# Optimization experiments

Hardware: AMD Instinct MI355X
Metric: run time of the kernel (lower is better)

## Reference

```python
import jax, jax.numpy as jnp
import numpy as np
import math

N_HEAD = 16

def _c(a):
    # stack real/imag -> complex64
    return jax.lax.complex(a[..., 0], a[..., 1])

def _rope_phasor(T, D, dtype=jnp.float32):
    inv_freq = 1.0 / (10000.0 ** (jnp.arange(D, dtype=dtype) / D))
    t = jnp.arange(T, dtype=dtype)
    freqs = jnp.outer(t, inv_freq)  # [T, D]
    return jax.lax.complex(jnp.cos(freqs), jnp.sin(freqs))

def setup_inputs() -> dict:
    key = jax.random.key(0)
    ks = jax.random.split(key, 9)
    B, T, C = 2, 1024, 1024
    s = 0.02
    return {
        "x":  jax.random.normal(ks[0], (B, T, C, 2), jnp.float32),
        "wq": jax.random.normal(ks[1], (C, C, 2), jnp.float32) * s,
        "bq": jax.random.normal(ks[2], (C, 2), jnp.float32) * s,
        "wk": jax.random.normal(ks[3], (C, C, 2), jnp.float32) * s,
        "bk": jax.random.normal(ks[4], (C, 2), jnp.float32) * s,
        "wv": jax.random.normal(ks[5], (C, C, 2), jnp.float32) * s,
        "bv": jax.random.normal(ks[6], (C, 2), jnp.float32) * s,
        "wo": jax.random.normal(ks[7], (C, C, 2), jnp.float32) * s,
        "bo": jax.random.normal(ks[8], (C, 2), jnp.float32) * s,
    }

def reference(x, wq, bq, wk, bk, wv, bv, wo, bo):
    B, T, C, _ = x.shape
    H = N_HEAD
    D = C // H
    xc = _c(x)
    # complex linear projections: y = x @ W^T + b
    q = xc @ _c(wq).T + _c(bq)
    k = xc @ _c(wk).T + _c(bk)
    v = xc @ _c(wv).T + _c(bv)
    # [B, T, C] -> [B, H, T, D]
    q = q.reshape(B, T, H, D).transpose(0, 2, 1, 3)
    k = k.reshape(B, T, H, D).transpose(0, 2, 1, 3)
    v = v.reshape(B, T, H, D).transpose(0, 2, 1, 3)
    # complex RoPE phasor multiply
    ph = _rope_phasor(T, D)[None, None]  # [1,1,T,D]
    q = q * ph
    k = k * ph
    # complex QK^H, scaled
    score = jnp.einsum('bhtd,bhsd->bhts', q, jnp.conj(k)) / math.sqrt(D)
    # softmax over magnitude, then real-valued complex weights
    attn = jax.nn.softmax(jnp.abs(score), axis=-1)
    attn_c = jax.lax.complex(attn, jnp.zeros_like(attn))
    out = jnp.einsum('bhts,bhsd->bhtd', attn_c, v)
    out = out.transpose(0, 2, 1, 3).reshape(B, T, C)
    out = out @ _c(wo).T + _c(bo)
    # return real/imag stacked for a real-valued harness
    return jnp.stack([out.real, out.imag], axis=-1)
```

## Files before the change

kernel.cpp:

```cpp
#include <hip/hip_runtime.h>
#include <math.h>

#define T_SEQ  1024
#define C_DIM  1024
#define NH_    16
#define H_DIM  64
#define SCL    (0.125f * 1.4426950408889634f)

typedef __bf16 bf16;
typedef __bf16 bf16x4 __attribute__((ext_vector_type(4)));
typedef __bf16 bf16x8 __attribute__((ext_vector_type(8)));
typedef float  f32x4  __attribute__((ext_vector_type(4)));

#define MFMA16(a, b, c) __builtin_amdgcn_mfma_f32_16x16x32_bf16(a, b, c, 0, 0, 0)

#define GLOAD_LDS16(g, l) __builtin_amdgcn_global_load_lds( \
    (const __attribute__((address_space(1))) void*)(g),     \
    (__attribute__((address_space(3))) void*)(l), 16, 0, 0)

__device__ __forceinline__ bf16x8 neg8(bf16x8 x) {
    union { bf16x8 v; unsigned int u[4]; } t;
    t.v = x;
    t.u[0] ^= 0x80008000u; t.u[1] ^= 0x80008000u;
    t.u[2] ^= 0x80008000u; t.u[3] ^= 0x80008000u;
    return t.v;
}

__device__ __forceinline__ bf16x8 frag_sw(const bf16* plane, int row, int chunk) {
    int c = chunk ^ (row & 7);
    return *(const bf16x8*)&plane[row * 64 + c * 8];
}
__device__ __forceinline__ bf16x8 frag_sw4(const bf16* plane, int row, int chunk) {
    int c = chunk ^ (row & 3);
    return *(const bf16x8*)&plane[row * 32 + c * 8];
}

__global__ __launch_bounds__(256)
void split_all(const float* __restrict__ x,  const float* __restrict__ wq,
               const float* __restrict__ wk, const float* __restrict__ wv,
               const float* __restrict__ wo,
               bf16* Xr, bf16* Xi, bf16* Wqr, bf16* Wqi, bf16* Wkr, bf16* Wki,
               bf16* Wvr, bf16* Wvi, bf16* Wor, bf16* Woi,
               float* __restrict__ rope)
{
    int z = blockIdx.y;
    if (z == 5) {
        if (blockIdx.x >= 256) return;
        int idx = blockIdx.x * 256 + threadIdx.x;
        int tp = idx >> 6, d = idx & 63;
        float invf = exp2f((float)d * -0.2076205059304601f);
        float fr = (float)tp * invf;
        float sn, cs; sincosf(fr, &sn, &cs);
        *(float2*)&rope[(size_t)idx * 2] = make_float2(cs, sn);
        return;
    }
    if (z > 0 && blockIdx.x >= 512) return;
    const float* in; bf16 *pr, *pi;
    if      (z == 0) { in = x;  pr = Xr;  pi = Xi;  }
    else if (z == 1) { in = wq; pr = Wqr; pi = Wqi; }
    else if (z == 2) { in = wk; pr = Wkr; pi = Wki; }
    else if (z == 3) { in = wv; pr = Wvr; pi = Wvi; }
    else             { in = wo; pr = Wor; pi = Woi; }
    int idx = (blockIdx.x * 256 + threadIdx.x) * 8;
    bf16x8 r, im;
#pragma unroll
    for (int j = 0; j < 4; j++) {
        float4 v = *(const float4*)(in + (size_t)idx * 2 + j * 4);
        r[2*j]   = (bf16)v.x; im[2*j]   = (bf16)v.y;
        r[2*j+1] = (bf16)v.z; im[2*j+1] = (bf16)v.w;
    }
    *(bf16x8*)(pr + idx) = r;
    *(bf16x8*)(pi + idx) = im;
}

__device__ __forceinline__ void cgemm128(
    bf16* __restrict__ smem,
    const bf16* __restrict__ Ar, const bf16* __restrict__ Ai,
    const bf16* __restrict__ Br, const bf16* __restrict__ Bi,
    const float* __restrict__ bias, const float* __restrict__ rope,
    bf16* __restrict__ Yr, bf16* __restrict__ Yi, int m0, int n0, int mode)
{
    const int t = threadIdx.x, lane = t & 63, wave = t >> 6;
    const int wm = (wave >> 1) * 64, wn = (wave & 1) * 32;
    const int lm = lane & 15, quad = lane >> 4;
    const int s_lr = lane >> 3, s_c = (lane & 7) ^ s_lr;

    f32x4 accr[4][2], acci[4][2];
#pragma unroll
    for (int i = 0; i < 4; i++)
#pragma unroll
        for (int j = 0; j < 2; j++) { accr[i][j] = (f32x4)0.f; acci[i][j] = (f32x4)0.f; }

    for (int k0 = 0; k0 < C_DIM; k0 += 64) {
#pragma unroll
        for (int j = 0; j < 12; j++) {
            int c = wave + 4 * j;
            const bf16* src; bf16* dst;
            if (c < 16)      {             src = Ar + (size_t)(m0 + c * 8 + s_lr) * C_DIM + k0 + s_c * 8; dst = smem + c * 512; }
            else if (c < 32) { int u = c - 16; src = Ai + (size_t)(m0 + u * 8 + s_lr) * C_DIM + k0 + s_c * 8; dst = smem + 8192 + u * 512; }
            else if (c < 40) { int u = c - 32; src = Br + (size_t)(n0 + u * 8 + s_lr) * C_DIM + k0 + s_c * 8; dst = smem + 16384 + u * 512; }
            else             { int u = c - 40; src = Bi + (size_t)(n0 + u * 8 + s_lr) * C_DIM + k0 + s_c * 8; dst = smem + 20480 + u * 512; }
            GLOAD_LDS16(src, dst);
        }
        __syncthreads();

#pragma unroll
        for (int kh = 0; kh < 2; kh++) {
            bf16x8 ar[4], ai_[4], br_[2], bi_[2], bn_[2];
#pragma unroll
            for (int i = 0; i < 4; i++) {
                ar[i]  = frag_sw(smem,        wm + i * 16 + lm, kh * 4 + quad);
                ai_[i] = frag_sw(smem + 8192, wm + i * 16 + lm, kh * 4 + quad);
            }
#pragma unroll
            for (int j = 0; j < 2; j++) {
                br_[j] = frag_sw(smem + 16384, wn + j * 16 + lm, kh * 4 + quad);
                bi_[j] = frag_sw(smem + 20480, wn + j * 16 + lm, kh * 4 + quad);
                bn_[j] = neg8(bi_[j]);
            }
#pragma unroll
            for (int i = 0; i < 4; i++)
#pragma unroll
                for (int j = 0; j < 2; j++) {
                    accr[i][j] = MFMA16(ar[i],  br_[j], accr[i][j]);
                    accr[i][j] = MFMA16(ai_[i], bn_[j], accr[i][j]);
                    acci[i][j] = MFMA16(ar[i],  bi_[j], acci[i][j]);
                    acci[i][j] = MFMA16(ai_[i], br_[j], acci[i][j]);
                }
        }
        __syncthreads();
    }

    const int h = n0 >> 6, bb = m0 >> 10, tbase = m0 & (T_SEQ - 1);

    if (mode == 1) {
#pragma unroll
        for (int i = 0; i < 4; i++)
#pragma unroll
            for (int j = 0; j < 2; j++) {
                int d = wn + j * 16 + lm;
                float2 bv = *(const float2*)&bias[2 * (n0 + d)];
#pragma unroll
                for (int r = 0; r < 4; r++) {
                    int tpos = tbase + wm + i * 16 + quad * 4 + r;
                    float2 ph = *(const float2*)&rope[((size_t)tpos * H_DIM + d) * 2];
                    float yr = accr[i][j][r] + bv.x;
                    float yi = acci[i][j][r] + bv.y;
                    accr[i][j][r] = yr * ph.x - yi * ph.y;
                    acci[i][j][r] = yr * ph.y + yi * ph.x;
                }
            }
        bf16* dsts[2] = { Yr, Yi };
#pragma unroll
        for (int pass = 0; pass < 2; pass++) {
            __syncthreads();
#pragma unroll
            for (int i = 0; i < 4; i++)
#pragma unroll
                for (int j = 0; j < 2; j++)
#pragma unroll
                    for (int r = 0; r < 4; r++)
                        smem[(wm + i * 16 + quad * 4 + r) * 72 + wn + j * 16 + lm] =
                            (bf16)(pass ? acci[i][j][r] : accr[i][j][r]);
            __syncthreads();
            bf16* dst = dsts[pass] + ((size_t)(bb * NH_ + h) * T_SEQ + tbase) * H_DIM;
#pragma unroll
            for (int p = 0; p < 4; p++) {
                int ch = t + 256 * p;
                int row = ch >> 3, o = (ch & 7) * 8;
                *(bf16x8*)&dst[row * H_DIM + o] = *(const bf16x8*)&smem[row * 72 + o];
            }
        }
    } else {
        bf16* dsts[2] = { Yr, Yi };
#pragma unroll
        for (int pass = 0; pass < 2; pass++) {
            __syncthreads();
#pragma unroll
            for (int i = 0; i < 4; i++)
#pragma unroll
                for (int j = 0; j < 2; j++) {
                    int d = wn + j * 16 + lm;
                    float2 bv = *(const float2*)&bias[2 * (n0 + d)];
                    float bb2 = pass ? bv.y : bv.x;
                    bf16x4 pk;
#pragma unroll
                    for (int r = 0; r < 4; r++)
                        pk[r] = (bf16)((pass ? acci[i][j][r] : accr[i][j][r]) + bb2);
                    *(bf16x4*)&smem[d * 136 + wm + i * 16 + quad * 4] = pk;
                }
            __syncthreads();
            bf16* dst = dsts[pass] + ((size_t)(bb * NH_ + h) * H_DIM) * T_SEQ + tbase;
#pragma unroll
            for (int p = 0; p < 4; p++) {
                int ch = t + 256 * p;
                int row = ch >> 4, o = (ch & 15) * 8;
                *(bf16x8*)&dst[(size_t)row * T_SEQ + o] = *(const bf16x8*)&smem[row * 136 + o];
            }
        }
    }
}

__global__ __launch_bounds__(256, 3)
void qkv_gemm(const bf16* __restrict__ Xr, const bf16* __restrict__ Xi,
              const bf16* __restrict__ Wqr, const bf16* __restrict__ Wqi,
              const bf16* __restrict__ Wkr, const bf16* __restrict__ Wki,
              const bf16* __restrict__ Wvr, const bf16* __restrict__ Wvi,
              const float* __restrict__ bq, const float* __restrict__ bk,
              const float* __restrict__ bv, const float* __restrict__ rope,
              bf16* Qr, bf16* Qi, bf16* Kr, bf16* Ki, bf16* Vr, bf16* Vi)
{
    __shared__ __attribute__((aligned(16))) bf16 smem[24576];
    int m0 = blockIdx.y * 128, n0 = blockIdx.x * 64;
    const bf16 *Br, *Bi; const float* bias; bf16 *Yr, *Yi; int mode;
    if (blockIdx.z == 0)      { Br = Wqr; Bi = Wqi; bias = bq; Yr = Qr; Yi = Qi; mode = 1; }
    else if (blockIdx.z == 1) { Br = Wkr; Bi = Wki; bias = bk; Yr = Kr; Yi = Ki; mode = 1; }
    else                      { Br = Wvr; Bi = Wvi; bias = bv; Yr = Vr; Yi = Vi; mode = 2; }
    cgemm128(smem, Xr, Xi, Br, Bi, bias, rope, Yr, Yi, m0, n0, mode);
}

__global__ __launch_bounds__(256, 4)
void out_gemm(const bf16* __restrict__ Ar, const bf16* __restrict__ Ai,
              const bf16* __restrict__ Br, const bf16* __restrict__ Bi,
              const float* __restrict__ bias, float* __restrict__ Y)
{
    __shared__ __attribute__((aligned(16))) bf16 sm[16384];
    const int t = threadIdx.x, lane = t & 63, wave = t >> 6;
    const int lm = lane & 15, quad = lane >> 4;
    const int s_lr = lane >> 3, s_c = (lane & 7) ^ s_lr;
    const int wm = (wave >> 1) * 32, wn = (wave & 1) * 32;
    const int m0 = blockIdx.y * 64, n0 = blockIdx.x * 64;

    f32x4 accr[2][2], acci[2][2];
#pragma unroll
    for (int i = 0; i < 2; i++)
#pragma unroll
        for (int j = 0; j < 2; j++) { accr[i][j] = (f32x4)0.f; acci[i][j] = (f32x4)0.f; }

    for (int k0 = 0; k0 < C_DIM; k0 += 64) {
#pragma unroll
        for (int j = 0; j < 8; j++) {
            int c = wave + 4 * j;
            const bf16* src; bf16* dst;
            if (c < 8)       {             src = Ar + (size_t)(m0 + c * 8 + s_lr) * C_DIM + k0 + s_c * 8; dst = sm + c * 512; }
            else if (c < 16) { int u = c - 8;  src = Ai + (size_t)(m0 + u * 8 + s_lr) * C_DIM + k0 + s_c * 8; dst = sm + 4096 + u * 512; }
            else if (c < 24) { int u = c - 16; src = Br + (size_t)(n0 + u * 8 + s_lr) * C_DIM + k0 + s_c * 8; dst = sm + 8192 + u * 512; }
            else             { int u = c - 24; src = Bi + (size_t)(n0 + u * 8 + s_lr) * C_DIM + k0 + s_c * 8; dst = sm + 12288 + u * 512; }
            GLOAD_LDS16(src, dst);
        }
        __syncthreads();
#pragma unroll
        for (int kh = 0; kh < 2; kh++) {
            bf16x8 ar[2], ai_[2], br_[2], bi_[2], bn_[2];
#pragma unroll
            for (int i = 0; i < 2; i++) {
                ar[i]  = frag_sw(sm,        wm + i * 16 + lm, kh * 4 + quad);
                ai_[i] = frag_sw(sm + 4096, wm + i * 16 + lm, kh * 4 + quad);
            }
#pragma unroll
            for (int j = 0; j < 2; j++) {
                br_[j] = frag_sw(sm + 8192,  wn + j * 16 + lm, kh * 4 + quad);
                bi_[j] = frag_sw(sm + 12288, wn + j * 16 + lm, kh * 4 + quad);
                bn_[j] = neg8(bi_[j]);
            }
#pragma unroll
            for (int i = 0; i < 2; i++)
#pragma unroll
                for (int j = 0; j < 2; j++) {
                    accr[i][j] = MFMA16(ar[i],  br_[j], accr[i][j]);
                    accr[i][j] = MFMA16(ai_[i], bn_[j], accr[i][j]);
                    acci[i][j] = MFMA16(ar[i],  bi_[j], acci[i][j]);
                    acci[i][j] = MFMA16(ai_[i], br_[j], acci[i][j]);
                }
        }
        __syncthreads();
    }
#pragma unroll
    for (int i = 0; i < 2; i++)
#pragma unroll
        for (int j = 0; j < 2; j++) {
            int n = n0 + wn + j * 16 + lm;
            float2 bv = *(const float2*)&bias[2 * n];
#pragma unroll
            for (int r = 0; r < 4; r++) {
                int m = m0 + wm + i * 16 + quad * 4 + r;
                *(float2*)&Y[((size_t)m * C_DIM + n) * 2] =
                    make_float2(accr[i][j][r] + bv.x, acci[i][j][r] + bv.y);
            }
        }
}

__global__ __launch_bounds__(512, 4)
void attn_mfma(const bf16* __restrict__ Qpr, const bf16* __restrict__ Qpi,
               const bf16* __restrict__ Kpr, const bf16* __restrict__ Kpi,
               const bf16* __restrict__ Vtr, const bf16* __restrict__ Vti,
               bf16* __restrict__ ABr, bf16* __restrict__ ABi)
{
    __shared__ __attribute__((aligned(16))) bf16 smem[32768];
    const int t = threadIdx.x, lane = t & 63, w = t >> 6;
    const int qg = w & 3, sh = w >> 2;
    const int lm = lane & 15, quad = lane >> 4;
    const int q0 = blockIdx.x * 64;
    const int h = blockIdx.y, b = blockIdx.z;
    const size_t hb = (size_t)(b * NH_ + h) * T_SEQ * H_DIM;
    const int s_lr = lane >> 3, s_c = (lane & 7) ^ s_lr;
    const int lr4 = lane >> 2, sc4 = ((lane & 3) ^ (lr4 & 3)) * 8;

    {
        const bf16* gq = (sh ? Qpi : Qpr) + hb + (size_t)q0 * H_DIM;
        bf16* lq = smem + 16384 + sh * 4096;
#pragma unroll
        for (int j = 0; j < 2; j++) {
            int cc = qg * 2 + j;
            GLOAD_LDS16(gq + (cc * 8 + s_lr) * H_DIM + s_c * 8, lq + cc * 512);
        }
    }
    __syncthreads();

    bf16x8 qfr[2], qfi[2], nqfr[2];
#pragma unroll
    for (int kh = 0; kh < 2; kh++) {
        qfr[kh]  = frag_sw(smem + 16384, qg * 16 + lm, kh * 4 + quad);
        qfi[kh]  = frag_sw(smem + 20480, qg * 16 + lm, kh * 4 + quad);
        nqfr[kh] = neg8(qfr[kh]);
    }

#pragma unroll
    for (int pre = 0; pre < 1; pre++) {
        const int S = sh * 512;
        bf16* bd = smem + sh * 8192;
        if (qg < 2) {
            const bf16* g = (qg ? Kpi : Kpr) + hb + (size_t)S * H_DIM;
            bf16* d = bd + (qg ? 2048 : 0);
#pragma unroll
            for (int cc = 0; cc < 4; cc++)
                GLOAD_LDS16(g + (cc * 8 + s_lr) * H_DIM + s_c * 8, d + cc * 512);
        } else {
            const bf16* g = (qg == 2 ? Vtr : Vti) + hb + S;
            bf16* d = bd + (qg == 2 ? 4096 : 6144);
#pragma unroll
            for (int cc = 0; cc < 4; cc++)
                GLOAD_LDS16(g + (size_t)(cc * 16 + lr4) * T_SEQ + sc4, d + cc * 512);
        }
    }

    f32x4 Or[4], Oi[4];
#pragma unroll
    for (int nt = 0; nt < 4; nt++) { Or[nt] = (f32x4)0.f; Oi[nt] = (f32x4)0.f; }
    float lsum = 0.f;
    const int idxA = (((2 * quad) & 3) * 16 + lm) * 4;
    const int idxB = idxA + 64;
    const bool hisel = quad >= 2;

    for (int it = 0; it < 16; it++) {
        __syncthreads();
        if (it < 15) {
            const int S = (it + 1) * 32 + sh * 512;
            bf16* bd = smem + ((it + 1) & 1) * 16384 + sh * 8192;
            if (qg < 2) {
                const bf16* g = (qg ? Kpi : Kpr) + hb + (size_t)S * H_DIM;
                bf16* d = bd + (qg ? 2048 : 0);
#pragma unroll
                for (int cc = 0; cc < 4; cc++)
                    GLOAD_LDS16(g + (cc * 8 + s_lr) * H_DIM + s_c * 8, d + cc * 512);
            } else {
                const bf16* g = (qg == 2 ? Vtr : Vti) + hb + S;
                bf16* d = bd + (qg == 2 ? 4096 : 6144);
#pragma unroll
                for (int cc = 0; cc < 4; cc++)
                    GLOAD_LDS16(g + (size_t)(cc * 16 + lr4) * T_SEQ + sc4, d + cc * 512);
            }
        }
        const bf16* buf = smem + (it & 1) * 16384 + sh * 8192;

        union { unsigned int u[2]; bf16 b[4]; } pk[2];
#pragma unroll
        for (int ct = 0; ct < 2; ct++) {
            f32x4 sre = (f32x4)0.f, sim = (f32x4)0.f;
#pragma unroll
            for (int kh = 0; kh < 2; kh++) {
                bf16x8 kr = frag_sw(buf,        ct * 16 + lm, kh * 4 + quad);
                bf16x8 ki = frag_sw(buf + 2048, ct * 16 + lm, kh * 4 + quad);
                sre = MFMA16(kr, qfr[kh],  sre);
                sre = MFMA16(ki, qfi[kh],  sre);
                sim = MFMA16(kr, qfi[kh],  sim);
                sim = MFMA16(ki, nqfr[kh], sim);
            }
#pragma unroll
            for (int r = 0; r < 4; r++) {
                float p = exp2f(sqrtf(sre[r] * sre[r] + sim[r] * sim[r]) * SCL);
                lsum += p;
                pk[ct].b[r] = (bf16)p;
            }
        }

        union { unsigned int u[4]; bf16x8 v; } pf;
        {
            int a0 = __builtin_amdgcn_ds_bpermute(idxA, (int)pk[0].u[0]);
            int a1 = __builtin_amdgcn_ds_bpermute(idxA, (int)pk[1].u[0]);
            int b0 = __builtin_amdgcn_ds_bpermute(idxA, (int)pk[0].u[1]);
            int b1 = __builtin_amdgcn_ds_bpermute(idxA, (int)pk[1].u[1]);
            int c0 = __builtin_amdgcn_ds_bpermute(idxB, (int)pk[0].u[0]);
            int c1 = __builtin_amdgcn_ds_bpermute(idxB, (int)pk[1].u[0]);
            int d0 = __builtin_amdgcn_ds_bpermute(idxB, (int)pk[0].u[1]);
            int d1 = __builtin_amdgcn_ds_bpermute(idxB, (int)pk[1].u[1]);
            pf.u[0] = (unsigned int)(hisel ? a1 : a0);
            pf.u[1] = (unsigned int)(hisel ? b1 : b0);
            pf.u[2] = (unsigned int)(hisel ? c1 : c0);
            pf.u[3] = (unsigned int)(hisel ? d1 : d0);
        }

#pragma unroll
        for (int nt = 0; nt < 4; nt++) {
            Or[nt] = MFMA16(pf.v, frag_sw4(buf + 4096, nt * 16 + lm, quad), Or[nt]);
            Oi[nt] = MFMA16(pf.v, frag_sw4(buf + 6144, nt * 16 + lm, quad), Oi[nt]);
        }
    }

    lsum += __shfl_xor(lsum, 16);
    lsum += __shfl_xor(lsum, 32);

    __syncthreads();
    float* Of  = (float*)smem;
    float* lsc = Of + 128 * 66;
    if (sh == 1) {
#pragma unroll
        for (int nt = 0; nt < 4; nt++)
#pragma unroll
            for (int r = 0; r < 4; r++) {
                Of[((qg * 2 + 0) * 16 + quad * 4 + r) * 66 + nt * 16 + lm] = Or[nt][r];
                Of[((qg * 2 + 1) * 16 + quad * 4 + r) * 66 + nt * 16 + lm] = Oi[nt][r];
            }
        if (quad == 0) lsc[qg * 16 + lm] = lsum;
    }
    __syncthreads();
    if (sh == 0) {
        float ltot = lsum + lsc[qg * 16 + lm];
        float lv = 1.f / ltot;
        float linv[4];
#pragma unroll
        for (int r = 0; r < 4; r++)
            linv[r] = __shfl(lv, (quad << 4) + quad * 4 + r, 64);
        size_t mbase = (size_t)(b * T_SEQ + q0 + qg * 16 + quad * 4) * C_DIM;
        int colb = h * H_DIM + lm;
#pragma unroll
        for (int nt = 0; nt < 4; nt++)
#pragma unroll
            for (int r = 0; r < 4; r++) {
                float orv = Or[nt][r] + Of[((qg * 2 + 0) * 16 + quad * 4 + r) * 66 + nt * 16 + lm];
                float oiv = Oi[nt][r] + Of[((qg * 2 + 1) * 16 + quad * 4 + r) * 66 + nt * 16 + lm];
                size_t o = mbase + (size_t)r * C_DIM + colb + nt * 16;
                ABr[o] = (bf16)(orv * linv[r]);
                ABi[o] = (bf16)(oiv * linv[r]);
            }
    }
}

extern "C" void kernel_launch(void* const* d_in, const int* in_sizes, int n_in,
                              void* d_out, int out_size, void* d_ws, size_t ws_size,
                              hipStream_t stream) {
    const float* x  = (const float*)d_in[0];
    const float* wq = (const float*)d_in[1];
    const float* bq = (const float*)d_in[2];
    const float* wk = (const float*)d_in[3];
    const float* bk = (const float*)d_in[4];
    const float* wv = (const float*)d_in[5];
    const float* bv = (const float*)d_in[6];
    const float* wo = (const float*)d_in[7];
    const float* bo = (const float*)d_in[8];

    float* rope = (float*)d_ws;
    bf16* w = (bf16*)(rope + 131072);
    const size_t MSZ = (size_t)2048 * 1024;
    const size_t WSZ = (size_t)1024 * 1024;
    const size_t PSZ = (size_t)2 * NH_ * T_SEQ * H_DIM;

    bf16 *Xr = w, *Xi = Xr + MSZ;
    bf16 *Wqr = Xi + MSZ,  *Wqi = Wqr + WSZ;
    bf16 *Wkr = Wqi + WSZ, *Wki = Wkr + WSZ;
    bf16 *Wvr = Wki + WSZ, *Wvi = Wvr + WSZ;
    bf16 *Wor = Wvi + WSZ, *Woi = Wor + WSZ;
    bf16 *Qr = Woi + WSZ, *Qi = Qr + PSZ;
    bf16 *Kr = Qi + PSZ,  *Ki = Kr + PSZ;
    bf16 *Vr = Ki + PSZ,  *Vi = Vr + PSZ;
    bf16 *ABr = Vi + PSZ, *ABi = ABr + MSZ;

    split_all<<<dim3(1024, 6), 256, 0, stream>>>(x, wq, wk, wv, wo,
        Xr, Xi, Wqr, Wqi, Wkr, Wki, Wvr, Wvi, Wor, Woi, rope);

    qkv_gemm<<<dim3(16, 16, 3), 256, 0, stream>>>(
        Xr, Xi, Wqr, Wqi, Wkr, Wki, Wvr, Wvi, bq, bk, bv, rope,
        Qr, Qi, Kr, Ki, Vr, Vi);

    attn_mfma<<<dim3(16, 16, 2), 512, 0, stream>>>(
        Qr, Qi, Kr, Ki, Vr, Vi, ABr, ABi);

    out_gemm<<<dim3(16, 32), 256, 0, stream>>>(ABr, ABi, Wor, Woi, bo, (float*)d_out);
}
```

Baseline: 217.0 us.

## Restructure attention into smaller blocks with 16-key tiles and K16 MFMA for PV

The attention kernel goes from 512-thread blocks over 64 queries to 256-thread blocks over 32 queries, doubling the grid, and now streams 16-key tiles over 32 iterations instead of 32-key tiles. The P·V product uses the 16x16x16 bf16 MFMA, so the probability fragment from the score MFMA feeds it directly and the ds_bpermute shuffle goes away. The softmax scale is folded into the Q RoPE phasor in the QKV GEMM epilogue, removing a multiply per score. The trade-off is more barriers and loop iterations per block and half as much K/V reuse per load.

After: 234.7 us. 8.1% more time.

```diff
diff --git a/kernel.cpp b/kernel.cpp
--- a/kernel.cpp
+++ b/kernel.cpp
@@ -10,9 +10,11 @@
 typedef __bf16 bf16;
 typedef __bf16 bf16x4 __attribute__((ext_vector_type(4)));
 typedef __bf16 bf16x8 __attribute__((ext_vector_type(8)));
+typedef short  s16x4  __attribute__((ext_vector_type(4)));
 typedef float  f32x4  __attribute__((ext_vector_type(4)));
 
-#define MFMA16(a, b, c) __builtin_amdgcn_mfma_f32_16x16x32_bf16(a, b, c, 0, 0, 0)
+#define MFMA16(a, b, c)  __builtin_amdgcn_mfma_f32_16x16x32_bf16(a, b, c, 0, 0, 0)
+#define MFMAK16(a, b, c) __builtin_amdgcn_mfma_f32_16x16x16bf16_1k(a, b, c, 0, 0, 0)
 
 #define GLOAD_LDS16(g, l) __builtin_amdgcn_global_load_lds( \
     (const __attribute__((address_space(1))) void*)(g),     \
@@ -29,10 +31,6 @@
 __device__ __forceinline__ bf16x8 frag_sw(const bf16* plane, int row, int chunk) {
     int c = chunk ^ (row & 7);
     return *(const bf16x8*)&plane[row * 64 + c * 8];
-}
-__device__ __forceinline__ bf16x8 frag_sw4(const bf16* plane, int row, int chunk) {
-    int c = chunk ^ (row & 3);
-    return *(const bf16x8*)&plane[row * 32 + c * 8];
 }
 
 __global__ __launch_bounds__(256)
@@ -78,7 +76,8 @@
     const bf16* __restrict__ Ar, const bf16* __restrict__ Ai,
     const bf16* __restrict__ Br, const bf16* __restrict__ Bi,
     const float* __restrict__ bias, const float* __restrict__ rope,
-    bf16* __restrict__ Yr, bf16* __restrict__ Yi, int m0, int n0, int mode)
+    bf16* __restrict__ Yr, bf16* __restrict__ Yi, int m0, int n0, int mode,
+    float qscale)
 {
     const int t = threadIdx.x, lane = t & 63, wave = t >> 6;
     const int wm = (wave >> 1) * 64, wn = (wave & 1) * 32;
@@ -144,10 +143,11 @@
                 for (int r = 0; r < 4; r++) {
                     int tpos = tbase + wm + i * 16 + quad * 4 + r;
                     float2 ph = *(const float2*)&rope[((size_t)tpos * H_DIM + d) * 2];
+                    float px = ph.x * qscale, py = ph.y * qscale;
                     float yr = accr[i][j][r] + bv.x;
                     float yi = acci[i][j][r] + bv.y;
-                    accr[i][j][r] = yr * ph.x - yi * ph.y;
-                    acci[i][j][r] = yr * ph.y + yi * ph.x;
+                    accr[i][j][r] = yr * px - yi * py;
+                    acci[i][j][r] = yr * py + yi * px;
                 }
             }
         bf16* dsts[2] = { Yr, Yi };
@@ -212,11 +212,11 @@
 {
     __shared__ __attribute__((aligned(16))) bf16 smem[24576];
     int m0 = blockIdx.y * 128, n0 = blockIdx.x * 64;
-    const bf16 *Br, *Bi; const float* bias; bf16 *Yr, *Yi; int mode;
-    if (blockIdx.z == 0)      { Br = Wqr; Bi = Wqi; bias = bq; Yr = Qr; Yi = Qi; mode = 1; }
-    else if (blockIdx.z == 1) { Br = Wkr; Bi = Wki; bias = bk; Yr = Kr; Yi = Ki; mode = 1; }
-    else                      { Br = Wvr; Bi = Wvi; bias = bv; Yr = Vr; Yi = Vi; mode = 2; }
-    cgemm128(smem, Xr, Xi, Br, Bi, bias, rope, Yr, Yi, m0, n0, mode);
+    const bf16 *Br, *Bi; const float* bias; bf16 *Yr, *Yi; int mode; float qs;
+    if (blockIdx.z == 0)      { Br = Wqr; Bi = Wqi; bias = bq; Yr = Qr; Yi = Qi; mode = 1; qs = SCL;  }
+    else if (blockIdx.z == 1) { Br = Wkr; Bi = Wki; bias = bk; Yr = Kr; Yi = Ki; mode = 1; qs = 1.0f; }
+    else                      { Br = Wvr; Bi = Wvi; bias = bv; Yr = Vr; Yi = Vi; mode = 2; qs = 1.0f; }
+    cgemm128(smem, Xr, Xi, Br, Bi, bias, rope, Yr, Yi, m0, n0, mode, qs);
 }
 
 __global__ __launch_bounds__(256, 4)
@@ -290,153 +290,122 @@
         }
 }
 
-__global__ __launch_bounds__(512, 4)
+__global__ __launch_bounds__(256, 5)
 void attn_mfma(const bf16* __restrict__ Qpr, const bf16* __restrict__ Qpi,
                const bf16* __restrict__ Kpr, const bf16* __restrict__ Kpi,
                const bf16* __restrict__ Vtr, const bf16* __restrict__ Vti,
                bf16* __restrict__ ABr, bf16* __restrict__ ABi)
 {
-    __shared__ __attribute__((aligned(16))) bf16 smem[32768];
-    const int t = threadIdx.x, lane = t & 63, w = t >> 6;
-    const int qg = w & 3, sh = w >> 2;
+    __shared__ __attribute__((aligned(16))) bf16 smem[16384];
+    const int t = threadIdx.x, lane = t & 63, wv = t >> 6;
+    const int qg = wv & 1, sh = wv >> 1;
     const int lm = lane & 15, quad = lane >> 4;
-    const int q0 = blockIdx.x * 64;
+    const int q0 = blockIdx.x * 32;
     const int h = blockIdx.y, b = blockIdx.z;
     const size_t hb = (size_t)(b * NH_ + h) * T_SEQ * H_DIM;
     const int s_lr = lane >> 3, s_c = (lane & 7) ^ s_lr;
-    const int lr4 = lane >> 2, sc4 = ((lane & 3) ^ (lr4 & 3)) * 8;
-
-    {
-        const bf16* gq = (sh ? Qpi : Qpr) + hb + (size_t)q0 * H_DIM;
-        bf16* lq = smem + 16384 + sh * 4096;
-#pragma unroll
-        for (int j = 0; j < 2; j++) {
-            int cc = qg * 2 + j;
-            GLOAD_LDS16(gq + (cc * 8 + s_lr) * H_DIM + s_c * 8, lq + cc * 512);
-        }
+
+#pragma unroll
+    for (int j = 0; j < 2; j++) {
+        int u = wv * 2 + j;
+        const bf16* gq = ((u >> 2) ? Qpi : Qpr) + hb + (size_t)q0 * H_DIM;
+        GLOAD_LDS16(gq + ((u & 3) * 8 + s_lr) * H_DIM + s_c * 8,
+                    smem + 8192 + (u >> 2) * 2048 + (u & 3) * 512);
     }
     __syncthreads();
-
     bf16x8 qfr[2], qfi[2], nqfr[2];
 #pragma unroll
     for (int kh = 0; kh < 2; kh++) {
-        qfr[kh]  = frag_sw(smem + 16384, qg * 16 + lm, kh * 4 + quad);
-        qfi[kh]  = frag_sw(smem + 20480, qg * 16 + lm, kh * 4 + quad);
+        qfr[kh]  = frag_sw(smem + 8192,  qg * 16 + lm, kh * 4 + quad);
+        qfi[kh]  = frag_sw(smem + 10240, qg * 16 + lm, kh * 4 + quad);
         nqfr[kh] = neg8(qfr[kh]);
     }
 
-#pragma unroll
-    for (int pre = 0; pre < 1; pre++) {
-        const int S = sh * 512;
-        bf16* bd = smem + sh * 8192;
-        if (qg < 2) {
-            const bf16* g = (qg ? Kpi : Kpr) + hb + (size_t)S * H_DIM;
-            bf16* d = bd + (qg ? 2048 : 0);
-#pragma unroll
-            for (int cc = 0; cc < 4; cc++)
-                GLOAD_LDS16(g + (cc * 8 + s_lr) * H_DIM + s_c * 8, d + cc * 512);
-        } else {
-            const bf16* g = (qg == 2 ? Vtr : Vti) + hb + S;
-            bf16* d = bd + (qg == 2 ? 4096 : 6144);
-#pragma unroll
-            for (int cc = 0; cc < 4; cc++)
-                GLOAD_LDS16(g + (size_t)(cc * 16 + lr4) * T_SEQ + sc4, d + cc * 512);
-        }
+    const bf16 *g0, *g1; size_t cstride; int gstep, dof0, dof1;
+    if (qg == 0) {
+        size_t off = hb + (size_t)(sh * 512) * H_DIM + (size_t)s_lr * H_DIM + s_c * 8;
+        g0 = Kpr + off; g1 = Kpi + off;
+        cstride = (size_t)8 * H_DIM; gstep = 16 * H_DIM;
+        dof0 = sh * 4096; dof1 = sh * 4096 + 1024;
+    } else {
+        size_t off = hb + (size_t)(sh * 512) + (size_t)(lane >> 1) * T_SEQ + (lane & 1) * 8;
+        g0 = Vtr + off; g1 = Vti + off;
+        cstride = (size_t)32 * T_SEQ; gstep = 16;
+        dof0 = sh * 4096 + 2048; dof1 = sh * 4096 + 3072;
+    }
+#pragma unroll
+    for (int cc = 0; cc < 2; cc++) {
+        GLOAD_LDS16(g0 + cc * cstride, smem + dof0 + cc * 512);
+        GLOAD_LDS16(g1 + cc * cstride, smem + dof1 + cc * 512);
     }
 
     f32x4 Or[4], Oi[4];
 #pragma unroll
     for (int nt = 0; nt < 4; nt++) { Or[nt] = (f32x4)0.f; Oi[nt] = (f32x4)0.f; }
     float lsum = 0.f;
-    const int idxA = (((2 * quad) & 3) * 16 + lm) * 4;
-    const int idxB = idxA + 64;
-    const bool hisel = quad >= 2;
-
-    for (int it = 0; it < 16; it++) {
+
+    for (int it = 0; it < 32; it++) {
         __syncthreads();
-        if (it < 15) {
-            const int S = (it + 1) * 32 + sh * 512;
-            bf16* bd = smem + ((it + 1) & 1) * 16384 + sh * 8192;
-            if (qg < 2) {
-                const bf16* g = (qg ? Kpi : Kpr) + hb + (size_t)S * H_DIM;
-                bf16* d = bd + (qg ? 2048 : 0);
-#pragma unroll
-                for (int cc = 0; cc < 4; cc++)
-                    GLOAD_LDS16(g + (cc * 8 + s_lr) * H_DIM + s_c * 8, d + cc * 512);
-            } else {
-                const bf16* g = (qg == 2 ? Vtr : Vti) + hb + S;
-                bf16* d = bd + (qg == 2 ? 4096 : 6144);
-#pragma unroll
-                for (int cc = 0; cc < 4; cc++)
-                    GLOAD_LDS16(g + (size_t)(cc * 16 + lr4) * T_SEQ + sc4, d + cc * 512);
-            }
-        }
-        const bf16* buf = smem + (it & 1) * 16384 + sh * 8192;
-
-        union { unsigned int u[2]; bf16 b[4]; } pk[2];
-#pragma unroll
-        for (int ct = 0; ct < 2; ct++) {
-            f32x4 sre = (f32x4)0.f, sim = (f32x4)0.f;
-#pragma unroll
-            for (int kh = 0; kh < 2; kh++) {
-                bf16x8 kr = frag_sw(buf,        ct * 16 + lm, kh * 4 + quad);
-                bf16x8 ki = frag_sw(buf + 2048, ct * 16 + lm, kh * 4 + quad);
-                sre = MFMA16(kr, qfr[kh],  sre);
-                sre = MFMA16(ki, qfi[kh],  sre);
-                sim = MFMA16(kr, qfi[kh],  sim);
-                sim = MFMA16(ki, nqfr[kh], sim);
-            }
-#pragma unroll
-            for (int r = 0; r < 4; r++) {
-                float p = exp2f(sqrtf(sre[r] * sre[r] + sim[r] * sim[r]) * SCL);
-                lsum += p;
-                pk[ct].b[r] = (bf16)p;
-            }
-        }
-
-        union { unsigned int u[4]; bf16x8 v; } pf;
-        {
-            int a0 = __builtin_amdgcn_ds_bpermute(idxA, (int)pk[0].u[0]);
-            int a1 = __builtin_amdgcn_ds_bpermute(idxA, (int)pk[1].u[0]);
-            int b0 = __builtin_amdgcn_ds_bpermute(idxA, (int)pk[0].u[1]);
-            int b1 = __builtin_amdgcn_ds_bpermute(idxA, (int)pk[1].u[1]);
-            int c0 = __builtin_amdgcn_ds_bpermute(idxB, (int)pk[0].u[0]);
-            int c1 = __builtin_amdgcn_ds_bpermute(idxB, (int)pk[1].u[0]);
-            int d0 = __builtin_amdgcn_ds_bpermute(idxB, (int)pk[0].u[1]);
-            int d1 = __builtin_amdgcn_ds_bpermute(idxB, (int)pk[1].u[1]);
-            pf.u[0] = (unsigned int)(hisel ? a1 : a0);
-            pf.u[1] = (unsigned int)(hisel ? b1 : b0);
-            pf.u[2] = (unsigned int)(hisel ? c1 : c0);
-            pf.u[3] = (unsigned int)(hisel ? d1 : d0);
-        }
-
+        if (it < 31) {
+            const bf16* s0 = g0 + (size_t)(it + 1) * gstep;
+            const bf16* s1 = g1 + (size_t)(it + 1) * gstep;
+            bf16* d = smem + ((it + 1) & 1) * 8192;
+#pragma unroll
+            for (int cc = 0; cc < 2; cc++) {
+                GLOAD_LDS16(s0 + cc * cstride, d + dof0 + cc * 512);
+                GLOAD_LDS16(s1 + cc * cstride, d + dof1 + cc * 512);
+            }
+        }
+        const bf16* buf = smem + (it & 1) * 8192 + sh * 4096;
+
+        f32x4 sre = (f32x4)0.f, sim = (f32x4)0.f;
+#pragma unroll
+        for (int kh = 0; kh < 2; kh++) {
+            bf16x8 kr = frag_sw(buf,        lm, kh * 4 + quad);
+            bf16x8 ki = frag_sw(buf + 1024, lm, kh * 4 + quad);
+            sre = MFMA16(kr, qfr[kh],  sre);
+            sre = MFMA16(ki, qfi[kh],  sre);
+            sim = MFMA16(kr, qfi[kh],  sim);
+            sim = MFMA16(ki, nqfr[kh], sim);
+        }
+        union { s16x4 s; bf16x4 b; } pf;
+#pragma unroll
+        for (int r = 0; r < 4; r++) {
+            float p = exp2f(sqrtf(sre[r] * sre[r] + sim[r] * sim[r]));
+            lsum += p;
+            pf.b[r] = (bf16)p;
+        }
+
+        const bf16* vr = buf + 2048;
+        const bf16* vi = buf + 3072;
 #pragma unroll
         for (int nt = 0; nt < 4; nt++) {
-            Or[nt] = MFMA16(pf.v, frag_sw4(buf + 4096, nt * 16 + lm, quad), Or[nt]);
-            Oi[nt] = MFMA16(pf.v, frag_sw4(buf + 6144, nt * 16 + lm, quad), Oi[nt]);
+            s16x4 vfr = *(const s16x4*)&vr[(nt * 16 + lm) * 16 + quad * 4];
+            s16x4 vfi = *(const s16x4*)&vi[(nt * 16 + lm) * 16 + quad * 4];
+            Or[nt] = MFMAK16(pf.s, vfr, Or[nt]);
+            Oi[nt] = MFMAK16(pf.s, vfi, Oi[nt]);
         }
     }
 
     lsum += __shfl_xor(lsum, 16);
     lsum += __shfl_xor(lsum, 32);
 
+    float* Of = (float*)smem;
+    float* fm = Of + 4096;
     __syncthreads();
-    float* Of  = (float*)smem;
-    float* lsc = Of + 128 * 66;
     if (sh == 1) {
 #pragma unroll
         for (int nt = 0; nt < 4; nt++)
 #pragma unroll
             for (int r = 0; r < 4; r++) {
-                Of[((qg * 2 + 0) * 16 + quad * 4 + r) * 66 + nt * 16 + lm] = Or[nt][r];
-                Of[((qg * 2 + 1) * 16 + quad * 4 + r) * 66 + nt * 16 + lm] = Oi[nt][r];
-            }
-        if (quad == 0) lsc[qg * 16 + lm] = lsum;
+                Of[(qg * 16 + quad * 4 + r) * 64 + nt * 16 + lm]        = Or[nt][r];
+                Of[(32 + qg * 16 + quad * 4 + r) * 64 + nt * 16 + lm]   = Oi[nt][r];
+            }
+        if (quad == 0) fm[qg * 16 + lm] = lsum;
     }
     __syncthreads();
     if (sh == 0) {
-        float ltot = lsum + lsc[qg * 16 + lm];
-        float lv = 1.f / ltot;
+        float lv = 1.f / (lsum + fm[qg * 16 + lm]);
         float linv[4];
 #pragma unroll
         for (int r = 0; r < 4; r++)
@@ -447,8 +416,8 @@
         for (int nt = 0; nt < 4; nt++)
 #pragma unroll
             for (int r = 0; r < 4; r++) {
-                float orv = Or[nt][r] + Of[((qg * 2 + 0) * 16 + quad * 4 + r) * 66 + nt * 16 + lm];
-                float oiv = Oi[nt][r] + Of[((qg * 2 + 1) * 16 + quad * 4 + r) * 66 + nt * 16 + lm];
+                float orv = Or[nt][r] + Of[(qg * 16 + quad * 4 + r) * 64 + nt * 16 + lm];
+                float oiv = Oi[nt][r] + Of[(32 + qg * 16 + quad * 4 + r) * 64 + nt * 16 + lm];
                 size_t o = mbase + (size_t)r * C_DIM + colb + nt * 16;
                 ABr[o] = (bf16)(orv * linv[r]);
                 ABi[o] = (bf16)(oiv * linv[r]);
@@ -492,7 +461,7 @@
         Xr, Xi, Wqr, Wqi, Wkr, Wki, Wvr, Wvi, bq, bk, bv, rope,
         Qr, Qi, Kr, Ki, Vr, Vi);
 
-    attn_mfma<<<dim3(16, 16, 2), 512, 0, stream>>>(
+    attn_mfma<<<dim3(32, 16, 2), 256, 0, stream>>>(
         Qr, Qi, Kr, Ki, Vr, Vi, ABr, ABi);
 
     out_gemm<<<dim3(16, 32), 256, 0, stream>>>(ABr, ABi, Wor, Woi, bo, (float*)d_out);
```
